# Kernel optimization log

Measured on AMD Instinct MI355X. Metric: run time of the kernel, lower is better.

## Reference

```python
import jax, jax.numpy as jnp
import numpy as np

B, T, N, FIN, FOUT, EDGE_DIM = 8, 16, 256, 32, 32, 16


def setup_inputs() -> dict:
    key = jax.random.key(0)
    ks = jax.random.split(key, 8)
    def xavier(k, shape):
        fan_in, fan_out = shape[0], shape[1]
        limit = float(np.sqrt(6.0 / (fan_in + fan_out)))
        return jax.random.uniform(k, shape, jnp.float32, -limit, limit)
    return {
        "x": jax.random.normal(ks[0], (B, T, N, FIN), jnp.float32),
        "adj": jax.random.uniform(ks[1], (N, N), jnp.float32),
        # edge_net: Linear(1, edge_dim) -> GELU -> Linear(edge_dim, Fin*Fout)
        "w1": xavier(ks[2], (1, EDGE_DIM)),
        "b1": jnp.zeros((EDGE_DIM,), jnp.float32),
        "w2": xavier(ks[3], (EDGE_DIM, FIN * FOUT)),
        "b2": jnp.zeros((FIN * FOUT,), jnp.float32),
        # node_lin: Linear(Fin, Fout)
        "node_w": xavier(ks[4], (FIN, FOUT)),
        "node_b": jnp.zeros((FOUT,), jnp.float32),
    }


def reference(x, adj, w1, b1, w2, b2, node_w, node_b):
    # edge-conditioned weights: (N, N, Fin, Fout)
    h = jax.nn.gelu(adj[:, :, None] * w1[0] + b1, approximate=False)  # (N,N,E)
    edge_w = (h @ w2 + b2).reshape(N, N, FIN, FOUT)
    # msg[b,t,i,j,:] = sum_f x[b,t,j,f] * edge_w[i,j,f,:]; agg = sum_j msg
    agg = jnp.einsum("btjf,ijfo->btio", x, edge_w)  # (B,T,N,Fout)
    y = jax.nn.gelu(x @ node_w + node_b + agg, approximate=False)
    return y
```

## Files before the change

kernel.cpp:

```cpp
#include <hip/hip_runtime.h>
#include <math.h>

#define NB    256
#define EDIM  16
#define FINN  32
#define FOUTN 32
#define BT    128
#define KKD   4096

typedef __attribute__((ext_vector_type(8))) short short8;
typedef __attribute__((ext_vector_type(4))) float floatx4;

#define MFMA16(a,b,c) __builtin_amdgcn_mfma_f32_16x16x32_bf16((a),(b),(c),0,0,0)

__device__ __forceinline__ float gelu_f(float v) {
    return 0.5f * v * (1.0f + erff(v * 0.70710678118654752f));
}
__device__ __forceinline__ ushort f2bf(float x) {
    union { float f; unsigned u; } v; v.f = x;
    unsigned r = (v.u + 0x7FFFu + ((v.u >> 16) & 1u)) >> 16;
    return (ushort)r;
}
__device__ __forceinline__ float bf2f(ushort b) {
    union { unsigned u; float f; } v; v.u = ((unsigned)b) << 16; return v.f;
}

__global__ __launch_bounds__(256) void h_kernel(const float* __restrict__ adj,
                                                const float* __restrict__ w1,
                                                const float* __restrict__ b1,
                                                ushort* __restrict__ H) {
    int i   = blockIdx.x;
    int tid = threadIdx.x;
    int e   = tid >> 4;
    int seg = tid & 15;
    float w = w1[e], b = b1[e];
    const float4* arow = (const float4*)(adj + (size_t)i * NB + seg * 16);
    ushort tmp[16];
    #pragma unroll
    for (int q = 0; q < 4; ++q) {
        float4 a = arow[q];
        tmp[q*4+0] = f2bf(gelu_f(a.x * w + b));
        tmp[q*4+1] = f2bf(gelu_f(a.y * w + b));
        tmp[q*4+2] = f2bf(gelu_f(a.z * w + b));
        tmp[q*4+3] = f2bf(gelu_f(a.w * w + b));
    }
    int4* dst = (int4*)(H + (size_t)i * KKD + e * 256 + seg * 16);
    dst[0] = *(int4*)&tmp[0];
    dst[1] = *(int4*)&tmp[8];
}

#define CH   256
#define NCH  16
#define BSP  264
#define XBP  40

__global__ __launch_bounds__(256, 2) void fused_kernel(
        const float* __restrict__ x,      const float* __restrict__ w2,
        const float* __restrict__ b2,     const float* __restrict__ node_w,
        const float* __restrict__ node_b, const ushort* __restrict__ H,
        float* __restrict__ out) {
    __shared__ ushort xb[NB][XBP];
    __shared__ ushort Bs[2][32][BSP];
    __shared__ ushort nwT[32][XBP];
    __shared__ float  Sp[8][32];
    __shared__ float  Sv[32];
    __shared__ float  bias2[32];

    int bt   = blockIdx.x;
    int iq   = blockIdx.y;
    int tid  = threadIdx.x;
    int wv   = tid >> 6;
    int lane = tid & 63;
    int m    = lane & 15;
    int quad = lane >> 4;

    const float4* xg = (const float4*)(x + (size_t)bt * NB * FINN);
    #pragma unroll
    for (int it = 0; it < 8; ++it) {
        int idx4 = it * 256 + tid;
        float4 v = xg[idx4];
        int j = idx4 >> 3, f = (idx4 & 7) * 4;
        unsigned lo = (unsigned)f2bf(v.x) | ((unsigned)f2bf(v.y) << 16);
        unsigned hi = (unsigned)f2bf(v.z) | ((unsigned)f2bf(v.w) << 16);
        uint2 p; p.x = lo; p.y = hi;
        *(uint2*)&xb[j][f] = p;
    }
    {
        float4 v = ((const float4*)node_w)[tid];
        int f = tid >> 3, o = (tid & 7) * 4;
        nwT[o + 0][f] = f2bf(v.x); nwT[o + 1][f] = f2bf(v.y);
        nwT[o + 2][f] = f2bf(v.z); nwT[o + 3][f] = f2bf(v.w);
    }
    __syncthreads();

    {
        int f = tid & 31, grp = tid >> 5;
        float s = 0.f;
        for (int j = grp * 32; j < grp * 32 + 32; ++j) s += bf2f(xb[j][f]);
        Sp[grp][f] = s;
    }

    short8 afr[4];
    #pragma unroll
    for (int t = 0; t < 4; ++t)
        afr[t] = *(short8*)&xb[(wv * 4 + t) * 16 + m][quad * 8];

    __syncthreads();
    if (tid < 32) {
        float s = 0.f;
        #pragma unroll
        for (int g = 0; g < 8; ++g) s += Sp[g][tid];
        Sv[tid] = s;
    }

    floatx4 acc[2] = {};
    int i0g = iq * 64 + wv * 16;

    #define WLOAD(e, d0, d1)                                                  \
    {                                                                         \
        const float* wp = w2 + (size_t)(e) * (FINN * FOUTN)                   \
                          + (quad * 8) * FOUTN + m;                           \
        _Pragma("unroll")                                                     \
        for (int i = 0; i < 8; ++i) {                                         \
            d0[i] = (short)f2bf(wp[i * FOUTN]);                               \
            d1[i] = (short)f2bf(wp[i * FOUTN + 16]);                          \
        }                                                                     \
    }

    #define PRODUCE(buf, wa, wb)                                              \
    {                                                                         \
        _Pragma("unroll")                                                     \
        for (int t = 0; t < 4; ++t) {                                         \
            floatx4 z = {0.f, 0.f, 0.f, 0.f};                                 \
            floatx4 d0 = MFMA16(afr[t], wa, z);                               \
            floatx4 d1 = MFMA16(afr[t], wb, z);                               \
            int col = (wv * 4 + t) * 16 + quad * 4;                           \
            uint2 p0, p1;                                                     \
            p0.x = (unsigned)f2bf(d0[0]) | ((unsigned)f2bf(d0[1]) << 16);     \
            p0.y = (unsigned)f2bf(d0[2]) | ((unsigned)f2bf(d0[3]) << 16);     \
            p1.x = (unsigned)f2bf(d1[0]) | ((unsigned)f2bf(d1[1]) << 16);     \
            p1.y = (unsigned)f2bf(d1[2]) | ((unsigned)f2bf(d1[3]) << 16);     \
            *(uint2*)&Bs[buf][     m][col] = p0;                              \
            *(uint2*)&Bs[buf][16 + m][col] = p1;                              \
        }                                                                     \
    }

    short8 wc0, wc1;
    WLOAD(0, wc0, wc1);
    PRODUCE(0, wc0, wc1);
    __syncthreads();
    if (tid < 32) {
        float bb = node_b[tid];
        #pragma unroll
        for (int f = 0; f < FINN; ++f) bb += Sv[f] * b2[f * FOUTN + tid];
        bias2[tid] = bb;
    }

    #pragma unroll
    for (int c = 0; c < NCH; ++c) {
        if (c < NCH - 1) {
            short8 wn0, wn1;
            WLOAD(c + 1, wn0, wn1);
            PRODUCE((c + 1) & 1, wn0, wn1);
        }
        const ushort* Hrow0 = H + (size_t)(i0g + m) * KKD + c * CH;
        #pragma unroll
        for (int kk = 0; kk < CH; kk += 32) {
            short8 a0 = *(const short8*)(Hrow0 + kk + quad * 8);
            short8 b0 = *(short8*)&Bs[c & 1][     m][kk + quad * 8];
            short8 b1 = *(short8*)&Bs[c & 1][16 + m][kk + quad * 8];
            acc[0] = MFMA16(a0, b0, acc[0]);
            acc[1] = MFMA16(a0, b1, acc[1]);
        }
        __syncthreads();
    }

    {
        short8 xa = *(short8*)&xb[i0g + m][quad * 8];
        #pragma unroll
        for (int tn = 0; tn < 2; ++tn) {
            short8 nb = *(short8*)&nwT[tn * 16 + m][quad * 8];
            acc[tn] = MFMA16(xa, nb, acc[tn]);
        }
    }
    #pragma unroll
    for (int tn = 0; tn < 2; ++tn) {
        int o = tn * 16 + m;
        float bz = bias2[o];
        #pragma unroll
        for (int r = 0; r < 4; ++r) {
            int row = i0g + quad * 4 + r;
            out[((size_t)bt * NB + row) * FOUTN + o] = gelu_f(acc[tn][r] + bz);
        }
    }
}

extern "C" void kernel_launch(void* const* d_in, const int* in_sizes, int n_in,
                              void* d_out, int out_size, void* d_ws, size_t ws_size,
                              hipStream_t stream) {
    const float* x      = (const float*)d_in[0];
    const float* adj    = (const float*)d_in[1];
    const float* w1     = (const float*)d_in[2];
    const float* b1     = (const float*)d_in[3];
    const float* w2     = (const float*)d_in[4];
    const float* b2     = (const float*)d_in[5];
    const float* node_w = (const float*)d_in[6];
    const float* node_b = (const float*)d_in[7];
    float* out = (float*)d_out;

    ushort* H = (ushort*)d_ws;

    hipLaunchKernelGGL(h_kernel, dim3(NB), dim3(256), 0, stream,
                       adj, w1, b1, H);
    hipLaunchKernelGGL(fused_kernel, dim3(BT, 4), dim3(256), 0, stream,
                       x, w2, b2, node_w, node_b, H, out);
}
```

Before: 112.0 us.

## Pre-swizzle H into MFMA fragment layout and software-pipeline loads with XOR-swizzled LDS

The H producer kernel now writes the GELU edge hidden values in per-lane MFMA fragment order, so the fused kernel can load A fragments with fully coalesced 16-byte loads. The fused kernel register-prefetches the next chunk's H fragments and raw w2 floats one iteration ahead, overlapping global loads with the produce/GEMM stages. The B tile in shared memory uses an XOR swizzle to avoid bank conflicts. The extra register arrays (areg 2x8 short8, wfl 2x16 floats) raise register pressure under launch_bounds(256,2), and the loop is restructured to produce chunk c while consuming chunk c-1.

```diff
diff --git a/kernel.cpp b/kernel.cpp
--- a/kernel.cpp
+++ b/kernel.cpp
@@ -28,25 +28,36 @@
 __global__ __launch_bounds__(256) void h_kernel(const float* __restrict__ adj,
                                                 const float* __restrict__ w1,
                                                 const float* __restrict__ b1,
-                                                ushort* __restrict__ H) {
-    int i   = blockIdx.x;
+                                                ushort* __restrict__ Hf) {
+    __shared__ float adjs[16][264];
+    __shared__ float w1s[16], b1s[16];
+    int it = blockIdx.x & 15;
+    int kq = blockIdx.x >> 4;
     int tid = threadIdx.x;
-    int e   = tid >> 4;
-    int seg = tid & 15;
-    float w = w1[e], b = b1[e];
-    const float4* arow = (const float4*)(adj + (size_t)i * NB + seg * 16);
-    ushort tmp[16];
+    if (tid < 16) { w1s[tid] = w1[tid]; b1s[tid] = b1[tid]; }
     #pragma unroll
     for (int q = 0; q < 4; ++q) {
-        float4 a = arow[q];
-        tmp[q*4+0] = f2bf(gelu_f(a.x * w + b));
-        tmp[q*4+1] = f2bf(gelu_f(a.y * w + b));
-        tmp[q*4+2] = f2bf(gelu_f(a.z * w + b));
-        tmp[q*4+3] = f2bf(gelu_f(a.w * w + b));
-    }
-    int4* dst = (int4*)(H + (size_t)i * KKD + e * 256 + seg * 16);
-    dst[0] = *(int4*)&tmp[0];
-    dst[1] = *(int4*)&tmp[8];
+        int u = q * 256 + tid;
+        int row = u >> 6, c4 = u & 63;
+        *(float4*)&adjs[row][c4 * 4] =
+            ((const float4*)(adj + ((size_t)it * 16 + row) * 256))[c4];
+    }
+    __syncthreads();
+    #pragma unroll
+    for (int q = 0; q < 4; ++q) {
+        int u = q * 256 + tid;
+        int ks = kq * 16 + (u >> 6);
+        int lane = u & 63;
+        int m = lane & 15, quad = lane >> 4;
+        int e = ks >> 3;
+        int j0 = (ks & 7) * 32 + quad * 8;
+        float w = w1s[e], b = b1s[e];
+        ushort tmp[8];
+        #pragma unroll
+        for (int d = 0; d < 8; ++d)
+            tmp[d] = f2bf(gelu_f(adjs[m][j0 + d] * w + b));
+        *(int4*)(Hf + (((size_t)it * 128 + ks) * 64 + lane) * 8) = *(int4*)tmp;
+    }
 }
 
 #define CH   256
@@ -57,7 +68,7 @@
 __global__ __launch_bounds__(256, 2) void fused_kernel(
         const float* __restrict__ x,      const float* __restrict__ w2,
         const float* __restrict__ b2,     const float* __restrict__ node_w,
-        const float* __restrict__ node_b, const ushort* __restrict__ H,
+        const float* __restrict__ node_b, const ushort* __restrict__ Hf,
         float* __restrict__ out) {
     __shared__ ushort xb[NB][XBP];
     __shared__ ushort Bs[2][32][BSP];
@@ -73,16 +84,42 @@
     int lane = tid & 63;
     int m    = lane & 15;
     int quad = lane >> 4;
+    int mu   = m & 7;
+    int it   = iq * 4 + wv;
+    int i0g  = it * 16;
+
+    const ushort* Hlane = Hf + ((size_t)it * 128) * 512 + lane * 8;
+
+    short8 areg[2][8];
+    float  wfl[2][16];
+
+    #define WLOADF(e, dst)                                                    \
+    {                                                                         \
+        const float* wp = w2 + (size_t)(e) * 1024 + quad * 256 + m;           \
+        _Pragma("unroll")                                                     \
+        for (int ii = 0; ii < 8; ++ii) {                                      \
+            dst[ii]     = wp[ii * 32];                                        \
+            dst[8 + ii] = wp[ii * 32 + 16];                                   \
+        }                                                                     \
+    }
+    #define ALOAD(dst, c)                                                     \
+    {                                                                         \
+        _Pragma("unroll")                                                     \
+        for (int kk = 0; kk < 8; ++kk)                                        \
+            dst[kk] = *(const short8*)(Hlane + ((c) * 8 + kk) * 512);         \
+    }
+
+    WLOADF(0, wfl[1]);
 
     const float4* xg = (const float4*)(x + (size_t)bt * NB * FINN);
     #pragma unroll
-    for (int it = 0; it < 8; ++it) {
-        int idx4 = it * 256 + tid;
+    for (int itr = 0; itr < 8; ++itr) {
+        int idx4 = itr * 256 + tid;
         float4 v = xg[idx4];
         int j = idx4 >> 3, f = (idx4 & 7) * 4;
-        unsigned lo = (unsigned)f2bf(v.x) | ((unsigned)f2bf(v.y) << 16);
-        unsigned hi = (unsigned)f2bf(v.z) | ((unsigned)f2bf(v.w) << 16);
-        uint2 p; p.x = lo; p.y = hi;
+        uint2 p;
+        p.x = (unsigned)f2bf(v.x) | ((unsigned)f2bf(v.y) << 16);
+        p.y = (unsigned)f2bf(v.z) | ((unsigned)f2bf(v.w) << 16);
         *(uint2*)&xb[j][f] = p;
     }
     {
@@ -112,21 +149,19 @@
         for (int g = 0; g < 8; ++g) s += Sp[g][tid];
         Sv[tid] = s;
     }
+    if (tid >= 32 && tid < 64) {
+    }
 
     floatx4 acc[2] = {};
-    int i0g = iq * 64 + wv * 16;
-
-    #define WLOAD(e, d0, d1)                                                  \
-    {                                                                         \
-        const float* wp = w2 + (size_t)(e) * (FINN * FOUTN)                   \
-                          + (quad * 8) * FOUTN + m;                           \
-        _Pragma("unroll")                                                     \
-        for (int i = 0; i < 8; ++i) {                                         \
-            d0[i] = (short)f2bf(wp[i * FOUTN]);                               \
-            d1[i] = (short)f2bf(wp[i * FOUTN + 16]);                          \
-        }                                                                     \
-    }
-
+
+    #define WCONV(src, wa, wb)                                                \
+    {                                                                         \
+        _Pragma("unroll")                                                     \
+        for (int ii = 0; ii < 8; ++ii) {                                      \
+            wa[ii] = (short)f2bf(src[ii]);                                    \
+            wb[ii] = (short)f2bf(src[8 + ii]);                                \
+        }                                                                     \
+    }
     #define PRODUCE(buf, wa, wb)                                              \
     {                                                                         \
         _Pragma("unroll")                                                     \
@@ -134,46 +169,51 @@
             floatx4 z = {0.f, 0.f, 0.f, 0.f};                                 \
             floatx4 d0 = MFMA16(afr[t], wa, z);                               \
             floatx4 d1 = MFMA16(afr[t], wb, z);                               \
-            int col = (wv * 4 + t) * 16 + quad * 4;                           \
+            int jt = wv * 4 + t;                                              \
+            int pc = (((jt * 2 + (quad >> 1)) ^ mu) << 3) + ((quad & 1) << 2);\
             uint2 p0, p1;                                                     \
             p0.x = (unsigned)f2bf(d0[0]) | ((unsigned)f2bf(d0[1]) << 16);     \
             p0.y = (unsigned)f2bf(d0[2]) | ((unsigned)f2bf(d0[3]) << 16);     \
             p1.x = (unsigned)f2bf(d1[0]) | ((unsigned)f2bf(d1[1]) << 16);     \
             p1.y = (unsigned)f2bf(d1[2]) | ((unsigned)f2bf(d1[3]) << 16);     \
-            *(uint2*)&Bs[buf][     m][col] = p0;                              \
-            *(uint2*)&Bs[buf][16 + m][col] = p1;                              \
-        }                                                                     \
-    }
-
-    short8 wc0, wc1;
-    WLOAD(0, wc0, wc1);
-    PRODUCE(0, wc0, wc1);
-    __syncthreads();
-    if (tid < 32) {
-        float bb = node_b[tid];
-        #pragma unroll
-        for (int f = 0; f < FINN; ++f) bb += Sv[f] * b2[f * FOUTN + tid];
-        bias2[tid] = bb;
-    }
-
+            *(uint2*)&Bs[buf][     m][pc] = p0;                               \
+            *(uint2*)&Bs[buf][16 + m][pc] = p1;                               \
+        }                                                                     \
+    }
+    #define GEMMC(buf, ar)                                                    \
+    {                                                                         \
+        _Pragma("unroll")                                                     \
+        for (int kk = 0; kk < 8; ++kk) {                                      \
+            int pc = (((kk * 4 + quad) ^ mu) << 3);                           \
+            short8 b0 = *(short8*)&Bs[buf][     m][pc];                       \
+            short8 b1 = *(short8*)&Bs[buf][16 + m][pc];                       \
+            acc[0] = MFMA16(ar[kk], b0, acc[0]);                              \
+            acc[1] = MFMA16(ar[kk], b1, acc[1]);                              \
+        }                                                                     \
+    }
+
+    bool did_bias = false;
     #pragma unroll
     for (int c = 0; c < NCH; ++c) {
-        if (c < NCH - 1) {
-            short8 wn0, wn1;
-            WLOAD(c + 1, wn0, wn1);
-            PRODUCE((c + 1) & 1, wn0, wn1);
-        }
-        const ushort* Hrow0 = H + (size_t)(i0g + m) * KKD + c * CH;
-        #pragma unroll
-        for (int kk = 0; kk < CH; kk += 32) {
-            short8 a0 = *(const short8*)(Hrow0 + kk + quad * 8);
-            short8 b0 = *(short8*)&Bs[c & 1][     m][kk + quad * 8];
-            short8 b1 = *(short8*)&Bs[c & 1][16 + m][kk + quad * 8];
-            acc[0] = MFMA16(a0, b0, acc[0]);
-            acc[1] = MFMA16(a0, b1, acc[1]);
+        ALOAD(areg[c & 1], c);
+        if (c < NCH - 1) WLOADF(c + 1, wfl[c & 1]);
+        {
+            short8 wa, wb;
+            WCONV(wfl[(c + 1) & 1], wa, wb);
+            PRODUCE(c & 1, wa, wb);
+        }
+        if (c > 0) {
+            GEMMC((c - 1) & 1, areg[(c - 1) & 1]);
+        } else if (tid < 32 && !did_bias) {
+            float bb = node_b[tid];
+            #pragma unroll
+            for (int f = 0; f < FINN; ++f) bb += Sv[f] * b2[f * FOUTN + tid];
+            bias2[tid] = bb;
+            did_bias = true;
         }
         __syncthreads();
     }
+    GEMMC((NCH - 1) & 1, areg[(NCH - 1) & 1]);
 
     {
         short8 xa = *(short8*)&xb[i0g + m][quad * 8];
@@ -208,10 +248,10 @@
     const float* node_b = (const float*)d_in[7];
     float* out = (float*)d_out;
 
-    ushort* H = (ushort*)d_ws;
-
-    hipLaunchKernelGGL(h_kernel, dim3(NB), dim3(256), 0, stream,
-                       adj, w1, b1, H);
+    ushort* Hf = (ushort*)d_ws;
+
+    hipLaunchKernelGGL(h_kernel, dim3(128), dim3(256), 0, stream,
+                       adj, w1, b1, Hf);
     hipLaunchKernelGGL(fused_kernel, dim3(BT, 4), dim3(256), 0, stream,
-                       x, w2, b2, node_w, node_b, H, out);
-}
+                       x, w2, b2, node_w, node_b, Hf, out);
+}
```

Result: no change. 114.2 us (+1.9%).
